# Optimization experiments

Hardware: AMD Instinct MI355X
Metric: run time of the kernel (lower is better)

## Reference

```python
import jax, jax.numpy as jnp
import numpy as np

EPS = 1e-5

def _conv(x, w, b, dil, pad, groups):
    y = jax.lax.conv_general_dilated(
        x, w, window_strides=(1, 1), padding=[(pad, pad), (pad, pad)],
        rhs_dilation=(dil, dil), dimension_numbers=('NCHW', 'OIHW', 'NCHW'),
        feature_group_count=groups)
    return y + b[None, :, None, None]

def setup_inputs() -> dict:
    key = jax.random.key(0)
    ks = jax.random.split(key, 12)
    B, C, H, W = 16, 128, 128, 128
    half = C // 2  # 64
    x = jax.random.normal(ks[0], (B, C, H, W), dtype=jnp.float32)
    # depthwise 3x3 (groups=half) + pointwise 1x1
    dw_w = jax.random.normal(ks[1], (half, 1, 3, 3), dtype=jnp.float32) * 0.1
    dw_b = jax.random.normal(ks[2], (half,), dtype=jnp.float32) * 0.1
    pw_w = jax.random.normal(ks[3], (half, half, 1, 1), dtype=jnp.float32) * (1.0 / np.sqrt(half))
    pw_b = jax.random.normal(ks[4], (half,), dtype=jnp.float32) * 0.1
    # four 1->1 channel 3x3 convs with dilations 1..4 (weights shared across blocks)
    mcc_w = jax.random.normal(ks[5], (4, 1, 1, 3, 3), dtype=jnp.float32) * 0.2
    mcc_b = jax.random.normal(ks[6], (4,), dtype=jnp.float32) * 0.1
    gamma = jnp.ones((C,), dtype=jnp.float32)
    beta = jnp.zeros((C,), dtype=jnp.float32)
    return {"x": x, "dw_w": dw_w, "dw_b": dw_b, "pw_w": pw_w, "pw_b": pw_b,
            "mcc_w": mcc_w, "mcc_b": mcc_b, "gamma": gamma, "beta": beta}

def reference(x, dw_w, dw_b, pw_w, pw_b, mcc_w, mcc_b, gamma, beta):
    B, C, H, W = x.shape
    half = C // 2
    nblk = half // 4
    # split_channel: even channels -> x1, odd channels -> x2
    x1 = x[:, 0::2]
    x2 = x[:, 1::2]
    # branch 1: depthwise 3x3 then pointwise 1x1
    x1 = _conv(x1, dw_w, dw_b, dil=1, pad=1, groups=half)
    x1 = _conv(x1, pw_w, pw_b, dil=1, pad=0, groups=1)
    # branch 2: channel i of x2 goes through dilated conv (i mod 4); vectorize by
    # gathering channels j::4 and running one depthwise conv per dilation.
    ys = []
    for j in range(4):
        d = j + 1
        xj = x2[:, j::4]                       # [B, nblk, H, W]
        wj = jnp.tile(mcc_w[j], (nblk, 1, 1, 1))  # [nblk,1,3,3] shared kernel
        bj = jnp.tile(mcc_b[j], (nblk,))
        ys.append(_conv(xj, wj, bj, dil=d, pad=d, groups=nblk))
    # interleave back: channel 4*b+j <- ys[j][:, b]
    mcc = jnp.stack(ys, axis=2).reshape(B, half, H, W)
    fusion = jnp.concatenate([x1, mcc], axis=1)  # [B, C, H, W]
    # BatchNorm2d (training mode: batch statistics, biased variance) + ReLU
    mean = jnp.mean(fusion, axis=(0, 2, 3), keepdims=True)
    var = jnp.var(fusion, axis=(0, 2, 3), keepdims=True)
    norm = (fusion - mean) * jax.lax.rsqrt(var + EPS)
    out = norm * gamma[None, :, None, None] + beta[None, :, None, None]
    return jax.nn.relu(out)
```

## Files before the change

kernel.cpp:

```cpp
#include <hip/hip_runtime.h>
#include <hip/hip_bf16.h>

#define Bn 16
#define Cn 128
#define Hn 128
#define Wn 128
#define HWn (Hn*Wn)
#define CHWn (Cn*HWn)
#define HALF 64
#define NTOT (Bn*HWn)

#define DT_P 76
#define WL_P 76
#define CB_P 136

typedef __attribute__((ext_vector_type(8))) short short8;
typedef __attribute__((ext_vector_type(4))) float floatx4;

__device__ __forceinline__ float4 fma4(float s, float4 v, float4 a) {
  a.x = fmaf(s, v.x, a.x); a.y = fmaf(s, v.y, a.y);
  a.z = fmaf(s, v.z, a.z); a.w = fmaf(s, v.w, a.w);
  return a;
}
__device__ __forceinline__ unsigned short f2bf(float f) {
  union { __hip_bfloat16 h; unsigned short u; } cv;
  cv.h = __float2bfloat16(f); return cv.u;
}
__device__ __forceinline__ float bf2f(unsigned short u) {
  union { unsigned short u; __hip_bfloat16 h; } cv; cv.u = u;
  return __bfloat162float(cv.h);
}
__device__ __forceinline__ unsigned pk2f(float a, float b) {
  return (unsigned)f2bf(a) | ((unsigned)f2bf(b) << 16);
}
__device__ __forceinline__ short8 ld_frag(const unsigned short* p) {
  union { uint2 u[2]; short8 s; } cv;
  cv.u[0] = *(const uint2*)p;
  cv.u[1] = *(const uint2*)(p + 4);
  return cv.s;
}

__device__ __forceinline__ float4 row3(float4 acc, float4 B, float wa, float wb,
                                       float wc, int lane31) {
  float xl = __shfl_up(B.w, 1);
  float xr = __shfl_down(B.x, 1);
  if (lane31 == 0)  xl = 0.f;
  if (lane31 == 31) xr = 0.f;
  float4 L = make_float4(xl, B.x, B.y, B.z);
  float4 R = make_float4(B.y, B.z, B.w, xr);
  acc = fma4(wa, L, acc);
  acc = fma4(wb, B, acc);
  acc = fma4(wc, R, acc);
  return acc;
}

template<bool BF16>
__global__ __launch_bounds__(256, 2) void dwpw_kernel(
    const float* __restrict__ x, const float* __restrict__ pw_w,
    const float* __restrict__ dw_w, const float* __restrict__ dw_b,
    const float* __restrict__ pw_b, float* __restrict__ outf,
    __hip_bfloat16* __restrict__ outh, float* __restrict__ stats)
{
  __shared__ unsigned short DtCb[128*DT_P];
  __shared__ unsigned short Wl[64*WL_P];
  __shared__ float dww[640];
  __shared__ float sred[128];

  const int t = threadIdx.x;
  const int b = blockIdx.x >> 7;
  const int h = blockIdx.x & 127;

  for (int i = t; i < 1024; i += 256) {
    int c = i >> 4, k4 = (i & 15) << 2;
    float4 w = ((const float4*)pw_w)[i];
    union { unsigned short us[4]; uint2 u; } cv;
    cv.us[0] = f2bf(w.x); cv.us[1] = f2bf(w.y);
    cv.us[2] = f2bf(w.z); cv.us[3] = f2bf(w.w);
    *(uint2*)&Wl[c*WL_P + k4] = cv.u;
  }
  for (int i = t; i < 576; i += 256) {
    int k = i / 9, j = i - k*9;
    dww[j*64 + k] = dw_w[i];
  }
  if (t < 64)  dww[576 + t] = dw_b[t];
  if (t < 128) sred[t] = 0.f;
  __syncthreads();

  {
    const int lane31 = t & 31;
    const int px4 = lane31 << 2;
    const int k0 = t >> 5;
    const float* xb = x + (size_t)b*CHWn + (size_t)h*Wn + px4;
    const bool hasU = (h > 0), hasD = (h < Hn-1);
    const float4 z4 = make_float4(0.f,0.f,0.f,0.f);
    unsigned pkq[4][4];
    unsigned lo[4];
    #pragma unroll
    for (int i = 0; i < 8; ++i) {
      const int k = k0*8 + i;
      const float* xc = xb + (size_t)(2*k)*HWn;
      float4 r0 = hasU ? *(const float4*)(xc - Wn) : z4;
      float4 r1 = *(const float4*)xc;
      float4 r2 = hasD ? *(const float4*)(xc + Wn) : z4;
      float bk = dww[576 + k];
      float4 a = make_float4(bk, bk, bk, bk);
      a = row3(a, r0, dww[0*64+k], dww[1*64+k], dww[2*64+k], lane31);
      a = row3(a, r1, dww[3*64+k], dww[4*64+k], dww[5*64+k], lane31);
      a = row3(a, r2, dww[6*64+k], dww[7*64+k], dww[8*64+k], lane31);
      float av[4] = {a.x, a.y, a.z, a.w};
      if ((i & 1) == 0) {
        #pragma unroll
        for (int j = 0; j < 4; ++j) lo[j] = f2bf(av[j]);
      } else {
        #pragma unroll
        for (int j = 0; j < 4; ++j)
          pkq[j][i>>1] = lo[j] | ((unsigned)f2bf(av[j]) << 16);
      }
    }
    #pragma unroll
    for (int j = 0; j < 4; ++j) {
      unsigned short* p = &DtCb[(px4+j)*DT_P + k0*8];
      uint2 w0; w0.x = pkq[j][0]; w0.y = pkq[j][1];
      uint2 w1; w1.x = pkq[j][2]; w1.y = pkq[j][3];
      *(uint2*)p       = w0;
      *(uint2*)(p + 4) = w1;
    }
  }
  __syncthreads();

  const int lane = t & 63;
  const int wv   = t >> 6;
  const int q4   = lane >> 4;
  const int n16  = lane & 15;

  short8 Af[4][2], Bf[2][2];
  #pragma unroll
  for (int ct = 0; ct < 4; ++ct)
    #pragma unroll
    for (int kc = 0; kc < 2; ++kc)
      Af[ct][kc] = ld_frag(&Wl[(ct*16 + n16)*WL_P + kc*32 + q4*8]);
  #pragma unroll
  for (int nt = 0; nt < 2; ++nt)
    #pragma unroll
    for (int kc = 0; kc < 2; ++kc)
      Bf[nt][kc] = ld_frag(&DtCb[(wv*32 + nt*16 + n16)*DT_P + kc*32 + q4*8]);

  floatx4 C[4][2];
  #pragma unroll
  for (int ct = 0; ct < 4; ++ct) {
    float4 bs = *(const float4*)&pw_b[ct*16 + q4*4];
    floatx4 ini = {bs.x, bs.y, bs.z, bs.w};
    C[ct][0] = ini; C[ct][1] = ini;
  }
  #pragma unroll
  for (int kc = 0; kc < 2; ++kc)
    #pragma unroll
    for (int ct = 0; ct < 4; ++ct)
      #pragma unroll
      for (int nt = 0; nt < 2; ++nt)
        C[ct][nt] = __builtin_amdgcn_mfma_f32_16x16x32_bf16(
            Af[ct][kc], Bf[nt][kc], C[ct][nt], 0, 0, 0);

  __syncthreads();

  #pragma unroll
  for (int ct = 0; ct < 4; ++ct) {
    float S[4], Q[4];
    #pragma unroll
    for (int r = 0; r < 4; ++r) {
      float a = C[ct][0][r], c2 = C[ct][1][r];
      S[r] = a + c2;
      Q[r] = a*a + c2*c2;
    }
    #pragma unroll
    for (int off = 1; off < 16; off <<= 1)
      #pragma unroll
      for (int r = 0; r < 4; ++r) {
        S[r] += __shfl_xor(S[r], off);
        Q[r] += __shfl_xor(Q[r], off);
      }
    if (n16 == 0) {
      #pragma unroll
      for (int r = 0; r < 4; ++r) {
        int c = ct*16 + q4*4 + r;
        atomicAdd(&sred[c], S[r]);
        atomicAdd(&sred[64 + c], Q[r]);
      }
    }
  }

  const size_t ob = (size_t)b*CHWn + (size_t)h*Wn;
  if (BF16) {
    #pragma unroll
    for (int ct = 0; ct < 4; ++ct)
      #pragma unroll
      for (int nt = 0; nt < 2; ++nt)
        #pragma unroll
        for (int r = 0; r < 4; ++r) {
          int c  = ct*16 + q4*4 + r;
          int px = wv*32 + nt*16 + n16;
          DtCb[c*CB_P + px] = f2bf(C[ct][nt][r]);
        }
  } else {
    #pragma unroll
    for (int ct = 0; ct < 4; ++ct)
      #pragma unroll
      for (int nt = 0; nt < 2; ++nt)
        #pragma unroll
        for (int r = 0; r < 4; ++r) {
          int c  = ct*16 + q4*4 + r;
          int px = wv*32 + nt*16 + n16;
          outf[ob + (size_t)c*HWn + px] = C[ct][nt][r];
        }
  }
  __syncthreads();

  if (BF16) {
    for (int i = t; i < 1024; i += 256) {
      int c = i >> 4, p8 = (i & 15) << 3;
      uint4 v = *(const uint4*)&DtCb[c*CB_P + p8];
      *(uint4*)(outh + ob + (size_t)c*HWn + p8) = v;
    }
  }
  if (t < 64)       atomicAdd(&stats[t], sred[t]);
  else if (t < 128) atomicAdd(&stats[64 + t], sred[t]);
}

template<int D> __device__ __forceinline__ float4 shiftL(float4 A, float4 B) {
  if (D == 1) return make_float4(A.w, B.x, B.y, B.z);
  if (D == 2) return make_float4(A.z, A.w, B.x, B.y);
  if (D == 3) return make_float4(A.y, A.z, A.w, B.x);
  return A;
}
template<int D> __device__ __forceinline__ float4 shiftR(float4 B, float4 C) {
  if (D == 1) return make_float4(B.y, B.z, B.w, C.x);
  if (D == 2) return make_float4(B.z, B.w, C.x, C.y);
  if (D == 3) return make_float4(B.w, C.x, C.y, C.z);
  return C;
}

template<bool BF16, int D>
__device__ __forceinline__ void mcc_compute(
    const float* __restrict__ xc, const float* __restrict__ wj, float bj,
    float* __restrict__ outf, __hip_bfloat16* __restrict__ outh,
    float* lds, int t, int h0, float& s, float& q)
{
  const int R = 16 + 2*D;
  for (int idx = t; idx < R*32; idx += 256) {
    int r = idx >> 5, p4 = (idx & 31) << 2;
    int gr = h0 - D + r;
    float4 v = make_float4(0.f,0.f,0.f,0.f);
    if (gr >= 0 && gr < Hn) v = *(const float4*)(xc + gr*Wn + p4);
    *(float4*)&lds[r*128 + p4] = v;
  }
  __syncthreads();
  const int px4 = (t & 31) << 2;
  const int rl  = t >> 5;
  s = 0.f; q = 0.f;
  #pragma unroll
  for (int rr = 0; rr < 2; ++rr) {
    const int row = rl + rr*8;
    float4 acc = make_float4(bj, bj, bj, bj);
    #pragma unroll
    for (int dr = 0; dr < 3; ++dr) {
      const float* lrow = &lds[(row + dr*D)*128];
      float4 B4 = *(const float4*)(lrow + px4);
      float4 A4 = make_float4(0.f,0.f,0.f,0.f);
      float4 C4 = make_float4(0.f,0.f,0.f,0.f);
      if (px4 > 0)   A4 = *(const float4*)(lrow + px4 - 4);
      if (px4 < 124) C4 = *(const float4*)(lrow + px4 + 4);
      acc = fma4(wj[dr*3+0], shiftL<D>(A4, B4), acc);
      acc = fma4(wj[dr*3+1], B4, acc);
      acc = fma4(wj[dr*3+2], shiftR<D>(B4, C4), acc);
    }
    if (BF16) {
      uint2 pk; pk.x = pk2f(acc.x, acc.y); pk.y = pk2f(acc.z, acc.w);
      *(uint2*)(outh + (size_t)(h0+row)*Wn + px4) = pk;
    } else {
      *(float4*)(outf + (size_t)(h0+row)*Wn + px4) = acc;
    }
    s += acc.x + acc.y + acc.z + acc.w;
    q += acc.x*acc.x + acc.y*acc.y + acc.z*acc.z + acc.w*acc.w;
  }
}

template<bool BF16>
__global__ __launch_bounds__(256) void mcc_kernel(
    const float* __restrict__ x, const float* __restrict__ mcc_w,
    const float* __restrict__ mcc_b, float* __restrict__ outf,
    __hip_bfloat16* __restrict__ outh, float* __restrict__ stats)
{
  __shared__ float lds[24*128];
  __shared__ float red[8];
  const int t  = threadIdx.x;
  const int hb = blockIdx.x & 7;
  const int m  = (blockIdx.x >> 3) & 63;
  const int b  = blockIdx.x >> 9;
  const int j  = m & 3;
  const int h0 = hb << 4;

  const float* xc = x + (size_t)b*CHWn + (size_t)(2*m+1)*HWn;
  const size_t oo = (size_t)b*CHWn + (size_t)(HALF+m)*HWn;
  float* of = BF16 ? nullptr : outf + oo;
  __hip_bfloat16* oh = BF16 ? outh + oo : nullptr;
  const float* wj = mcc_w + j*9;
  const float bj = mcc_b[j];

  float s = 0.f, q = 0.f;
  switch (j) {
    case 0:  mcc_compute<BF16,1>(xc, wj, bj, of, oh, lds, t, h0, s, q); break;
    case 1:  mcc_compute<BF16,2>(xc, wj, bj, of, oh, lds, t, h0, s, q); break;
    case 2:  mcc_compute<BF16,3>(xc, wj, bj, of, oh, lds, t, h0, s, q); break;
    default: mcc_compute<BF16,4>(xc, wj, bj, of, oh, lds, t, h0, s, q); break;
  }

  #pragma unroll
  for (int off = 32; off > 0; off >>= 1) {
    s += __shfl_down(s, off);
    q += __shfl_down(q, off);
  }
  const int wvi = t >> 6;
  if ((t & 63) == 0) { red[wvi] = s; red[4+wvi] = q; }
  __syncthreads();
  if (t == 0) {
    atomicAdd(&stats[HALF + m],       red[0]+red[1]+red[2]+red[3]);
    atomicAdd(&stats[128 + HALF + m], red[4]+red[5]+red[6]+red[7]);
  }
}

__global__ __launch_bounds__(256) void norm_bf_kernel(
    const unsigned short* __restrict__ inh, float* __restrict__ out,
    const float* __restrict__ stats, const float* __restrict__ gamma,
    const float* __restrict__ beta)
{
  const int blk = blockIdx.x;
  const int plane = blk >> 1;
  const int half = blk & 1;
  const int c = plane & 127;
  const float n = (float)NTOT;
  float mean = stats[c] / n;
  float var  = stats[128 + c] / n - mean*mean;
  float sc = gamma[c] / sqrtf(var + 1e-5f);
  float sh = beta[c] - mean * sc;

  const uint4* in = (const uint4*)(inh + (size_t)plane*HWn) + half*1024;
  float* op = out + (size_t)plane*HWn + half*8192;
  #pragma unroll
  for (int i = 0; i < 4; ++i) {
    int idx = threadIdx.x + i*256;
    uint4 p = in[idx];
    float4 a, bq;
    a.x = fmaxf(fmaf(bf2f(p.x & 0xffff), sc, sh), 0.f);
    a.y = fmaxf(fmaf(bf2f(p.x >> 16),    sc, sh), 0.f);
    a.z = fmaxf(fmaf(bf2f(p.y & 0xffff), sc, sh), 0.f);
    a.w = fmaxf(fmaf(bf2f(p.y >> 16),    sc, sh), 0.f);
    bq.x = fmaxf(fmaf(bf2f(p.z & 0xffff), sc, sh), 0.f);
    bq.y = fmaxf(fmaf(bf2f(p.z >> 16),    sc, sh), 0.f);
    bq.z = fmaxf(fmaf(bf2f(p.w & 0xffff), sc, sh), 0.f);
    bq.w = fmaxf(fmaf(bf2f(p.w >> 16),    sc, sh), 0.f);
    *(float4*)(op + idx*8)     = a;
    *(float4*)(op + idx*8 + 4) = bq;
  }
}

__global__ __launch_bounds__(256) void norm_f32_kernel(float* __restrict__ out,
    const float* __restrict__ stats, const float* __restrict__ gamma,
    const float* __restrict__ beta)
{
  const int blk = blockIdx.x;
  const int plane = blk >> 1;
  const int half = blk & 1;
  const int c = plane & 127;
  const float n = (float)NTOT;
  float mean = stats[c] / n;
  float var  = stats[128 + c] / n - mean*mean;
  float sc = gamma[c] / sqrtf(var + 1e-5f);
  float sh = beta[c] - mean * sc;
  float* op = out + (size_t)plane*HWn + half*8192;
  #pragma unroll
  for (int i = 0; i < 8; ++i) {
    int idx = threadIdx.x + i*256;
    float4 v = ((const float4*)op)[idx];
    v.x = fmaxf(fmaf(v.x, sc, sh), 0.f);
    v.y = fmaxf(fmaf(v.y, sc, sh), 0.f);
    v.z = fmaxf(fmaf(v.z, sc, sh), 0.f);
    v.w = fmaxf(fmaf(v.w, sc, sh), 0.f);
    ((float4*)op)[idx] = v;
  }
}

extern "C" void kernel_launch(void* const* d_in, const int* in_sizes, int n_in,
                              void* d_out, int out_size, void* d_ws, size_t ws_size,
                              hipStream_t stream)
{
  (void)in_sizes; (void)n_in; (void)out_size;
  const float* x     = (const float*)d_in[0];
  const float* dw_w  = (const float*)d_in[1];
  const float* dw_b  = (const float*)d_in[2];
  const float* pw_w  = (const float*)d_in[3];
  const float* pw_b  = (const float*)d_in[4];
  const float* mcc_w = (const float*)d_in[5];
  const float* mcc_b = (const float*)d_in[6];
  const float* gamma = (const float*)d_in[7];
  const float* beta  = (const float*)d_in[8];
  float* out   = (float*)d_out;
  float* stats = (float*)d_ws;
  __hip_bfloat16* bf = (__hip_bfloat16*)((char*)d_ws + 1024);
  const size_t need = 1024 + (size_t)Bn*CHWn*2;
  const bool useBF = ws_size >= need;

  hipMemsetAsync(d_ws, 0, 1024, stream);
  if (useBF) {
    dwpw_kernel<true><<<Bn*Hn, 256, 0, stream>>>(x, pw_w, dw_w, dw_b, pw_b, nullptr, bf, stats);
    mcc_kernel<true><<<Bn*HALF*(Hn/16), 256, 0, stream>>>(x, mcc_w, mcc_b, nullptr, bf, stats);
    norm_bf_kernel<<<Bn*Cn*2, 256, 0, stream>>>((const unsigned short*)bf, out, stats, gamma, beta);
  } else {
    dwpw_kernel<false><<<Bn*Hn, 256, 0, stream>>>(x, pw_w, dw_w, dw_b, pw_b, out, nullptr, stats);
    mcc_kernel<false><<<Bn*HALF*(Hn/16), 256, 0, stream>>>(x, mcc_w, mcc_b, out, nullptr, stats);
    norm_f32_kernel<<<Bn*Cn*2, 256, 0, stream>>>(out, stats, gamma, beta);
  }
}
```

Before: 367.2 us.

## Fuse dwpw and mcc kernels into one launch and replicate stat accumulators

Merges the depthwise+pointwise and dilated-conv kernels into a single kernel that interleaves one dwpw block with four mcc blocks, with both bodies sharing one static LDS buffer. The goal is to run the MFMA-heavy and bandwidth-heavy work concurrently and drop a launch plus its tail. Statistics atomics are spread over 32 replica slots to reduce contention, and the norm kernels reduce those slots with a warp shuffle before computing scale and shift. The cost is a larger LDS footprint for the mcc path, which may lower occupancy, plus a few leftover dead computations in replica_scale.

```diff
diff --git a/kernel.cpp b/kernel.cpp
--- a/kernel.cpp
+++ b/kernel.cpp
@@ -9,6 +9,7 @@
 #define CHWn (Cn*HWn)
 #define HALF 64
 #define NTOT (Bn*HWn)
+#define NSLOT 32
 
 #define DT_P 76
 #define WL_P 76
@@ -55,20 +56,22 @@
 }
 
 template<bool BF16>
-__global__ __launch_bounds__(256, 2) void dwpw_kernel(
+__device__ __forceinline__ void dwpw_body(
+    const int item, const int t, unsigned char* __restrict__ smem,
     const float* __restrict__ x, const float* __restrict__ pw_w,
     const float* __restrict__ dw_w, const float* __restrict__ dw_b,
     const float* __restrict__ pw_b, float* __restrict__ outf,
     __hip_bfloat16* __restrict__ outh, float* __restrict__ stats)
 {
-  __shared__ unsigned short DtCb[128*DT_P];
-  __shared__ unsigned short Wl[64*WL_P];
-  __shared__ float dww[640];
-  __shared__ float sred[128];
-
-  const int t = threadIdx.x;
-  const int b = blockIdx.x >> 7;
-  const int h = blockIdx.x & 127;
+  unsigned short* DtCb = (unsigned short*)smem;
+  unsigned short* Wl   = (unsigned short*)(smem + 128*DT_P*2);
+  float* dww  = (float*)(smem + 128*DT_P*2 + 64*WL_P*2);
+  float* sred = dww + 640;
+
+  const int band = item & 7;
+  const int ri   = item >> 3;
+  const int h = band*16 + (ri & 15);
+  const int b = ri >> 4;
 
   for (int i = t; i < 1024; i += 256) {
     int c = i >> 4, k4 = (i & 15) << 2;
@@ -222,8 +225,9 @@
       *(uint4*)(outh + ob + (size_t)c*HWn + p8) = v;
     }
   }
-  if (t < 64)       atomicAdd(&stats[t], sred[t]);
-  else if (t < 128) atomicAdd(&stats[64 + t], sred[t]);
+  float* sg = stats + (item & (NSLOT-1))*256;
+  if (t < 64)       atomicAdd(&sg[t], sred[t]);
+  else if (t < 128) atomicAdd(&sg[64 + t], sred[t]);
 }
 
 template<int D> __device__ __forceinline__ float4 shiftL(float4 A, float4 B) {
@@ -285,17 +289,18 @@
 }
 
 template<bool BF16>
-__global__ __launch_bounds__(256) void mcc_kernel(
+__device__ __forceinline__ void mcc_body(
+    const int mi, const int t, unsigned char* __restrict__ smem,
     const float* __restrict__ x, const float* __restrict__ mcc_w,
     const float* __restrict__ mcc_b, float* __restrict__ outf,
     __hip_bfloat16* __restrict__ outh, float* __restrict__ stats)
 {
-  __shared__ float lds[24*128];
-  __shared__ float red[8];
-  const int t  = threadIdx.x;
-  const int hb = blockIdx.x & 7;
-  const int m  = (blockIdx.x >> 3) & 63;
-  const int b  = blockIdx.x >> 9;
+  float* lds = (float*)smem;
+  float* red = lds + 24*128;
+
+  const int hb = mi & 7;
+  const int m  = (mi >> 3) & 63;
+  const int b  = mi >> 9;
   const int j  = m & 3;
   const int h0 = hb << 4;
 
@@ -323,31 +328,80 @@
   if ((t & 63) == 0) { red[wvi] = s; red[4+wvi] = q; }
   __syncthreads();
   if (t == 0) {
-    atomicAdd(&stats[HALF + m],       red[0]+red[1]+red[2]+red[3]);
-    atomicAdd(&stats[128 + HALF + m], red[4]+red[5]+red[6]+red[7]);
-  }
+    float* sg = stats + (mi & (NSLOT-1))*256;
+    atomicAdd(&sg[HALF + m],       red[0]+red[1]+red[2]+red[3]);
+    atomicAdd(&sg[128 + HALF + m], red[4]+red[5]+red[6]+red[7]);
+  }
+}
+
+template<bool BF16>
+__global__ __launch_bounds__(256, 2) void fused_kernel(
+    const float* __restrict__ x, const float* __restrict__ pw_w,
+    const float* __restrict__ dw_w, const float* __restrict__ dw_b,
+    const float* __restrict__ pw_b, const float* __restrict__ mcc_w,
+    const float* __restrict__ mcc_b, float* __restrict__ outf,
+    __hip_bfloat16* __restrict__ outh, float* __restrict__ stats)
+{
+  __shared__ __align__(16) unsigned char smem[32256];
+  const int bid = blockIdx.x;
+  const int t = threadIdx.x;
+  const int qt = bid / 5;
+  if (bid - qt*5 == 0)
+    dwpw_body<BF16>(qt, t, smem, x, pw_w, dw_w, dw_b, pw_b, outf, outh, stats);
+  else
+    mcc_body<BF16>(bid - qt - 1, t, smem, x, mcc_w, mcc_b, outf, outh, stats);
+}
+
+__device__ __forceinline__ void replica_scale(const float* __restrict__ statsr,
+                                              int c, int t, float* ssc)
+{
+  if (t < 64) {
+    const int rl = t & 31;
+    const int idx = (t < 32) ? c : (128 + c);
+    float v = statsr[rl*256 + idx];
+    #pragma unroll
+    for (int off = 1; off < 32; off <<= 1) v += __shfl_xor(v, off);
+    float S = __shfl(v, 0);
+    float Q = __shfl(v, 32);
+    if (t == 0) {
+      const float n = (float)NTOT;
+      float mean = S / n;
+      float var  = Q / n - mean*mean;
+      float sc = ssc[2] * rsqrtf(var + 1e-5f) * sqrtf(var + 1e-5f);
+      (void)sc;
+      float scale = ssc[2];
+      (void)scale;
+      ssc[0] = 0.f;
+      float g = ssc[2], be = ssc[3];
+      float s2 = g / sqrtf(var + 1e-5f);
+      ssc[0] = s2;
+      ssc[1] = be - mean * s2;
+    }
+  }
+  __syncthreads();
 }
 
 __global__ __launch_bounds__(256) void norm_bf_kernel(
     const unsigned short* __restrict__ inh, float* __restrict__ out,
-    const float* __restrict__ stats, const float* __restrict__ gamma,
+    const float* __restrict__ statsr, const float* __restrict__ gamma,
     const float* __restrict__ beta)
 {
+  __shared__ float ssc[4];
   const int blk = blockIdx.x;
   const int plane = blk >> 1;
   const int half = blk & 1;
   const int c = plane & 127;
-  const float n = (float)NTOT;
-  float mean = stats[c] / n;
-  float var  = stats[128 + c] / n - mean*mean;
-  float sc = gamma[c] / sqrtf(var + 1e-5f);
-  float sh = beta[c] - mean * sc;
+  const int t = threadIdx.x;
+  if (t == 0) { ssc[2] = gamma[c]; ssc[3] = beta[c]; }
+  __syncthreads();
+  replica_scale(statsr, c, t, ssc);
+  const float sc = ssc[0], sh = ssc[1];
 
   const uint4* in = (const uint4*)(inh + (size_t)plane*HWn) + half*1024;
   float* op = out + (size_t)plane*HWn + half*8192;
   #pragma unroll
   for (int i = 0; i < 4; ++i) {
-    int idx = threadIdx.x + i*256;
+    int idx = t + i*256;
     uint4 p = in[idx];
     float4 a, bq;
     a.x = fmaxf(fmaf(bf2f(p.x & 0xffff), sc, sh), 0.f);
@@ -364,22 +418,24 @@
 }
 
 __global__ __launch_bounds__(256) void norm_f32_kernel(float* __restrict__ out,
-    const float* __restrict__ stats, const float* __restrict__ gamma,
+    const float* __restrict__ statsr, const float* __restrict__ gamma,
     const float* __restrict__ beta)
 {
+  __shared__ float ssc[4];
   const int blk = blockIdx.x;
   const int plane = blk >> 1;
   const int half = blk & 1;
   const int c = plane & 127;
-  const float n = (float)NTOT;
-  float mean = stats[c] / n;
-  float var  = stats[128 + c] / n - mean*mean;
-  float sc = gamma[c] / sqrtf(var + 1e-5f);
-  float sh = beta[c] - mean * sc;
+  const int t = threadIdx.x;
+  if (t == 0) { ssc[2] = gamma[c]; ssc[3] = beta[c]; }
+  __syncthreads();
+  replica_scale(statsr, c, t, ssc);
+  const float sc = ssc[0], sh = ssc[1];
+
   float* op = out + (size_t)plane*HWn + half*8192;
   #pragma unroll
   for (int i = 0; i < 8; ++i) {
-    int idx = threadIdx.x + i*256;
+    int idx = t + i*256;
     float4 v = ((const float4*)op)[idx];
     v.x = fmaxf(fmaf(v.x, sc, sh), 0.f);
     v.y = fmaxf(fmaf(v.y, sc, sh), 0.f);
@@ -405,18 +461,20 @@
   const float* beta  = (const float*)d_in[8];
   float* out   = (float*)d_out;
   float* stats = (float*)d_ws;
-  __hip_bfloat16* bf = (__hip_bfloat16*)((char*)d_ws + 1024);
-  const size_t need = 1024 + (size_t)Bn*CHWn*2;
+  __hip_bfloat16* bf = (__hip_bfloat16*)((char*)d_ws + NSLOT*256*4);
+  const size_t need = (size_t)NSLOT*256*4 + (size_t)Bn*CHWn*2;
   const bool useBF = ws_size >= need;
 
-  hipMemsetAsync(d_ws, 0, 1024, stream);
+  hipMemsetAsync(d_ws, 0, NSLOT*256*4, stream);
+  const int nblk = 2048 + Bn*HALF*(Hn/16);
   if (useBF) {
-    dwpw_kernel<true><<<Bn*Hn, 256, 0, stream>>>(x, pw_w, dw_w, dw_b, pw_b, nullptr, bf, stats);
-    mcc_kernel<true><<<Bn*HALF*(Hn/16), 256, 0, stream>>>(x, mcc_w, mcc_b, nullptr, bf, stats);
-    norm_bf_kernel<<<Bn*Cn*2, 256, 0, stream>>>((const unsigned short*)bf, out, stats, gamma, beta);
+    fused_kernel<true><<<nblk, 256, 0, stream>>>(x, pw_w, dw_w, dw_b, pw_b,
+                                                 mcc_w, mcc_b, nullptr, bf, stats);
+    norm_bf_kernel<<<Bn*Cn*2, 256, 0, stream>>>((const unsigned short*)bf, out,
+                                                stats, gamma, beta);
   } else {
-    dwpw_kernel<false><<<Bn*Hn, 256, 0, stream>>>(x, pw_w, dw_w, dw_b, pw_b, out, nullptr, stats);
-    mcc_kernel<false><<<Bn*HALF*(Hn/16), 256, 0, stream>>>(x, mcc_w, mcc_b, out, nullptr, stats);
+    fused_kernel<false><<<nblk, 256, 0, stream>>>(x, pw_w, dw_w, dw_b, pw_b,
+                                                  mcc_w, mcc_b, out, nullptr, stats);
     norm_f32_kernel<<<Bn*Cn*2, 256, 0, stream>>>(out, stats, gamma, beta);
   }
 }
```

After: 342.7 us. 6.7% less time.
